# Performance work log

Hardware: AMD Instinct MI355X
Metric: run time of the kernel (lower is better)

## Reference

```python
import jax, jax.numpy as jnp
import numpy as np

N, E = 20000, 640000
ND, ED = 16, 8            # raw node/edge feature dims
H = 128                   # encoder hidden = gnn channels = mlp hidden
OUT = 2
L = 10                    # gnn layers (shared weights, per-layer layernorms)
NOISE_STD = 0.003
EPS = 1e-5


def _mlp(x, w1, b1, w2, b2):
    return jax.nn.relu(x @ w1 + b1) @ w2 + b2


def _ln(x, g, b):
    m = jnp.mean(x, axis=-1, keepdims=True)
    v = jnp.var(x, axis=-1, keepdims=True)
    return (x - m) * jax.lax.rsqrt(v + EPS) * g + b


def setup_inputs() -> dict:
    key = jax.random.key(0)
    ks = jax.random.split(key, 32)

    def w(k, i, o):
        return jax.random.normal(k, (i, o), jnp.float32) / np.sqrt(i)

    inp = {
        "x": jax.random.normal(ks[0], (N, ND), jnp.float32),
        "edge_attr": jax.random.normal(ks[1], (E, ED), jnp.float32),
        "edge_index": jax.random.randint(ks[2], (2, E), 0, N, jnp.int64),
        "node_noise": jax.random.normal(ks[3], (N, ND), jnp.float32) * NOISE_STD,
        "edge_noise": jax.random.normal(ks[4], (E, ED), jnp.float32) * NOISE_STD,
        # encoders
        "node_enc_w1": w(ks[5], ND, H), "node_enc_b1": jnp.zeros((H,), jnp.float32),
        "node_enc_w2": w(ks[6], H, H),  "node_enc_b2": jnp.zeros((H,), jnp.float32),
        "edge_enc_w1": w(ks[7], ED, H), "edge_enc_b1": jnp.zeros((H,), jnp.float32),
        "edge_enc_w2": w(ks[8], H, H),  "edge_enc_b2": jnp.zeros((H,), jnp.float32),
        # single shared MPNN (module instance reused across all L layers)
        "gnn_edge_w1": w(ks[9], 3 * H, H), "gnn_edge_b1": jnp.zeros((H,), jnp.float32),
        "gnn_edge_w2": w(ks[10], H, H),    "gnn_edge_b2": jnp.zeros((H,), jnp.float32),
        "gnn_node_w1": w(ks[11], 2 * H, H), "gnn_node_b1": jnp.zeros((H,), jnp.float32),
        "gnn_node_w2": w(ks[12], H, H),     "gnn_node_b2": jnp.zeros((H,), jnp.float32),
        # per-layer layernorms
        "x_ln_g": jnp.ones((L, H), jnp.float32), "x_ln_b": jnp.zeros((L, H), jnp.float32),
        "e_ln_g": jnp.ones((L, H), jnp.float32), "e_ln_b": jnp.zeros((L, H), jnp.float32),
        # decoder
        "dec_w1": w(ks[13], H, H),  "dec_b1": jnp.zeros((H,), jnp.float32),
        "dec_w2": w(ks[14], H, OUT), "dec_b2": jnp.zeros((OUT,), jnp.float32),
    }
    return inp


def reference(x, edge_attr, edge_index, node_noise, edge_noise,
              node_enc_w1, node_enc_b1, node_enc_w2, node_enc_b2,
              edge_enc_w1, edge_enc_b1, edge_enc_w2, edge_enc_b2,
              gnn_edge_w1, gnn_edge_b1, gnn_edge_w2, gnn_edge_b2,
              gnn_node_w1, gnn_node_b1, gnn_node_w2, gnn_node_b2,
              x_ln_g, x_ln_b, e_ln_g, e_ln_b,
              dec_w1, dec_b1, dec_w2, dec_b2):
    src = edge_index[0]  # x_j
    dst = edge_index[1]  # x_i (aggregation target)

    h = _mlp(x + node_noise, node_enc_w1, node_enc_b1, node_enc_w2, node_enc_b2)      # [N,H]
    e = _mlp(edge_attr + edge_noise, edge_enc_w1, edge_enc_b1, edge_enc_w2, edge_enc_b2)  # [E,H]

    for l in range(L):
        xi = h[dst]  # [E,H]
        xj = h[src]  # [E,H]
        # edge update: e + edge_mlp([x_i, x_j, e])
        e_new = e + _mlp(jnp.concatenate([xi, xj, e], axis=1),
                         gnn_edge_w1, gnn_edge_b1, gnn_edge_w2, gnn_edge_b2)
        # message: x_i + node_mlp([x_i, e_new]); aggr='add' over dst
        msg = xi + _mlp(jnp.concatenate([xi, e_new], axis=1),
                        gnn_node_w1, gnn_node_b1, gnn_node_w2, gnn_node_b2)
        h_agg = jax.ops.segment_sum(msg, dst, num_segments=N)
        h = _ln(h + h_agg, x_ln_g[l], x_ln_b[l])
        e = _ln(e + e_new, e_ln_g[l], e_ln_b[l])

    out = _mlp(h, dec_w1, dec_b1, dec_w2, dec_b2) - node_noise[:, :OUT]
    return out
```

## Files before the change

### kernel.cpp

```cpp
#include <hip/hip_runtime.h>
#include <stdio.h>

#define NN 20000
#define NE 640000
#define NL 10

typedef unsigned short u16;
typedef unsigned int u32;
typedef __attribute__((ext_vector_type(8))) __bf16 bf16x8;
typedef __attribute__((ext_vector_type(8))) unsigned short us8;
typedef __attribute__((ext_vector_type(4))) float f32x4;

__device__ __forceinline__ bf16x8 ldbf(const u16* p) {
  union { us8 u; bf16x8 b; } v;
  v.u = *(const us8*)p;
  return v.b;
}
__device__ __forceinline__ f32x4 zero4() {
  f32x4 z; z[0] = 0.f; z[1] = 0.f; z[2] = 0.f; z[3] = 0.f; return z;
}
__device__ __forceinline__ float bf2f(u16 u) {
  u32 x = ((u32)u) << 16;
  return __uint_as_float(x);
}
__device__ __forceinline__ u16 f2bf(float f) {
  u32 x = __float_as_uint(f);
  u32 r = (x + 0x7fffu + ((x >> 16) & 1u)) >> 16;
  return (u16)r;
}
__device__ __forceinline__ int lad(int row, int col) {
  return (row << 7) + ((((col >> 3) ^ (row & 15)) << 3) | (col & 7));
}
__device__ __forceinline__ uint2 pack4bf(const float f[4]) {
  uint2 u;
  u.x = (u32)f2bf(f[0]) | ((u32)f2bf(f[1]) << 16);
  u.y = (u32)f2bf(f[2]) | ((u32)f2bf(f[3]) << 16);
  return u;
}
__device__ __forceinline__ void unpack4bf(uint2 u, float f[4]) {
  f[0] = bf2f((u16)(u.x & 0xffffu)); f[1] = bf2f((u16)(u.x >> 16));
  f[2] = bf2f((u16)(u.y & 0xffffu)); f[3] = bf2f((u16)(u.y >> 16));
}

__global__ void LearnedSimModel_28716151341396_kernel() {}

__global__ void init_kernel(float* agg, int agg_n, int* cnt, int cnt_n) {
  int i = blockIdx.x * 256 + threadIdx.x;
  if (i < agg_n) agg[i] = 0.0f;
  if (i < cnt_n) cnt[i] = 0;
}

__global__ void idx_detect_kernel(const int* raw, int* flag) {
  if (threadIdx.x == 0 && blockIdx.x == 0) {
    int any = 0;
    for (int k = 0; k < 16; ++k) any = any | raw[2 * k + 1];
    flag[0] = (any != 0) ? 1 : 0;
  }
}

__global__ void idx_prep_kernel(const int* raw, const int* flag, int* idx0) {
  int i = blockIdx.x * 256 + threadIdx.x;
  if (i < 2 * NE) {
    int v;
    if (flag[0] != 0) v = raw[i];
    else v = (int)(((const long long*)raw)[i]);
    if (v < 0) v = 0;
    if (v >= NN) v = NN - 1;
    idx0[i] = v;
  }
}

__global__ void hist_kernel(const int* dst0, int* cnt) {
  int i = blockIdx.x * 256 + threadIdx.x;
  if (i < NE) atomicAdd(&cnt[dst0[i]], 1);
}

__global__ void prefix_kernel(const int* cnt, int* cursor) {
  __shared__ int buf[1024];
  __shared__ int carry;
  int t = threadIdx.x;
  if (t == 0) carry = 0;
  __syncthreads();
  for (int base = 0; base < NN; base += 1024) {
    int v = (base + t < NN) ? cnt[base + t] : 0;
    buf[t] = v;
    __syncthreads();
    for (int s = 1; s < 1024; s <<= 1) {
      int add = (t >= s) ? buf[t - s] : 0;
      __syncthreads();
      buf[t] += add;
      __syncthreads();
    }
    int excl = buf[t] - v + carry;
    if (base + t < NN) cursor[base + t] = excl;
    __syncthreads();
    if (t == 0) carry = carry + buf[1023];
    __syncthreads();
  }
}

__global__ void scatter_kernel(const int* src0, const int* dst0, int* cursor,
                               int* src_s, int* dst_s, int* perm) {
  int i = blockIdx.x * 256 + threadIdx.x;
  if (i < NE) {
    int d = dst0[i];
    int pos = atomicAdd(&cursor[d], 1);
    perm[pos] = i;
    src_s[pos] = src0[i];
    dst_s[pos] = d;
  }
}

__global__ void transpose_slice_kernel(const float* __restrict__ W,
                                       u16* __restrict__ Wt, int koff) {
  int i = blockIdx.x * 256 + threadIdx.x;
  int k = i >> 7, f = i & 127;
  Wt[f * 128 + k] = f2bf(W[(size_t)(koff + k) * 128 + f]);
}

__global__ void node_enc_kernel(const float* x, const float* noise,
                                const float* w1, const float* b1,
                                const float* w2, const float* b2,
                                float* h, u16* h16) {
  __shared__ float in16[16];
  __shared__ float t1s[128];
  int f = threadIdx.x;
  int n = blockIdx.x;
  if (f < 16) in16[f] = x[n * 16 + f] + noise[n * 16 + f];
  __syncthreads();
  float a = b1[f];
  for (int k = 0; k < 16; ++k) a += in16[k] * w1[k * 128 + f];
  t1s[f] = fmaxf(a, 0.0f);
  __syncthreads();
  float o = b2[f];
  for (int k = 0; k < 128; ++k) o += t1s[k] * w2[k * 128 + f];
  h[(long long)n * 128 + f] = o;
  h16[(long long)n * 128 + f] = f2bf(o);
}

__device__ __forceinline__ void gemm128(const u16* lds, const u16* Wt,
                                        int l16, int quad, int fb, f32x4 acc[2][4]) {
  for (int ks = 0; ks < 4; ++ks) {
    int kg = ks * 32 + quad * 8;
    bf16x8 b0 = ldbf(lds + lad(0 * 16 + l16, kg));
    bf16x8 b1 = ldbf(lds + lad(1 * 16 + l16, kg));
    bf16x8 b2 = ldbf(lds + lad(2 * 16 + l16, kg));
    bf16x8 b3 = ldbf(lds + lad(3 * 16 + l16, kg));
    for (int tt = 0; tt < 2; ++tt) {
      bf16x8 a = ldbf(Wt + (size_t)(fb + tt * 16 + l16) * 128 + kg);
      acc[tt][0] = __builtin_amdgcn_mfma_f32_16x16x32_bf16(a, b0, acc[tt][0], 0, 0, 0);
      acc[tt][1] = __builtin_amdgcn_mfma_f32_16x16x32_bf16(a, b1, acc[tt][1], 0, 0, 0);
      acc[tt][2] = __builtin_amdgcn_mfma_f32_16x16x32_bf16(a, b2, acc[tt][2], 0, 0, 0);
      acc[tt][3] = __builtin_amdgcn_mfma_f32_16x16x32_bf16(a, b3, acc[tt][3], 0, 0, 0);
    }
  }
}

__global__ __launch_bounds__(256) void edge_enc_mfma(
    const float* __restrict__ attr, const float* __restrict__ noise,
    const int* __restrict__ perm,
    const float* __restrict__ w1, const float* __restrict__ b1,
    const u16* __restrict__ Wt2, const float* __restrict__ b2,
    u16* __restrict__ e)
{
  __shared__ __align__(16) u16 sT[64 * 128];
  __shared__ float sIn[64][8];
  __shared__ int sPerm[64];

  const int t = threadIdx.x;
  if (t < 64) sPerm[t] = perm[blockIdx.x * 64 + t];
  __syncthreads();

  for (int it = 0; it < 2; ++it) {
    int c = t + it * 256;
    int row = c >> 3, k = c & 7;
    int p = sPerm[row];
    sIn[row][k] = attr[(size_t)p * 8 + k] + noise[(size_t)p * 8 + k];
  }
  __syncthreads();

  {
    int f = t & 127;
    int r0 = (t >> 7) * 32;
    float wc[8];
    for (int k = 0; k < 8; ++k) wc[k] = w1[k * 128 + f];
    float bb = b1[f];
    for (int j = 0; j < 32; ++j) {
      int row = r0 + j;
      float a = bb;
      for (int k = 0; k < 8; ++k) a += sIn[row][k] * wc[k];
      sT[lad(row, f)] = f2bf(fmaxf(a, 0.f));
    }
  }
  __syncthreads();

  const int lane = t & 63;
  const int wave = t >> 6;
  const int l16 = lane & 15;
  const int quad = lane >> 4;
  const int fb = wave * 32;
  f32x4 acc[2][4];
  for (int tt = 0; tt < 2; ++tt)
    for (int et = 0; et < 4; ++et) acc[tt][et] = zero4();
  gemm128(sT, Wt2, l16, quad, fb, acc);
  u16* etile = e + (size_t)blockIdx.x * 8192;
  for (int tt = 0; tt < 2; ++tt) {
    int f0 = fb + tt * 16 + quad * 4;
    float4 bb = *(const float4*)(b2 + f0);
    float bbv[4] = {bb.x, bb.y, bb.z, bb.w};
    for (int et = 0; et < 4; ++et) {
      int row = et * 16 + l16;
      float o[4];
      for (int r = 0; r < 4; ++r) o[r] = acc[tt][et][r] + bbv[r];
      *(uint2*)(etile + lad(row, f0)) = pack4bf(o);
    }
  }
}

__global__ __launch_bounds__(256) void nprep_kernel(
    const u16* __restrict__ h16, const u16* __restrict__ Wt_np,
    float* __restrict__ nprep)
{
  __shared__ __align__(16) u16 sH[64 * 128];
  const int t = threadIdx.x;
  const int n0 = blockIdx.x * 64;

  for (int it = 0; it < 4; ++it) {
    int c = t + it * 256;
    int row = c >> 4, seg = c & 15;
    int n = n0 + row;
    if (n >= NN) n = NN - 1;
    us8 v = *(const us8*)(h16 + (size_t)n * 128 + seg * 8);
    *(us8*)(sH + ((row << 7) + ((seg ^ (row & 15)) << 3))) = v;
  }
  __syncthreads();

  const int lane = t & 63;
  const int wave = t >> 6;
  const int l16 = lane & 15;
  const int quad = lane >> 4;
  const int fb = wave * 96;
  f32x4 acc[6][4];
  for (int ft = 0; ft < 6; ++ft)
    for (int et = 0; et < 4; ++et) acc[ft][et] = zero4();
  for (int ks = 0; ks < 4; ++ks) {
    int kg = ks * 32 + quad * 8;
    bf16x8 b0 = ldbf(sH + lad(0 * 16 + l16, kg));
    bf16x8 b1 = ldbf(sH + lad(1 * 16 + l16, kg));
    bf16x8 b2 = ldbf(sH + lad(2 * 16 + l16, kg));
    bf16x8 b3 = ldbf(sH + lad(3 * 16 + l16, kg));
    for (int ft = 0; ft < 6; ++ft) {
      bf16x8 a = ldbf(Wt_np + (size_t)(fb + ft * 16 + l16) * 128 + kg);
      acc[ft][0] = __builtin_amdgcn_mfma_f32_16x16x32_bf16(a, b0, acc[ft][0], 0, 0, 0);
      acc[ft][1] = __builtin_amdgcn_mfma_f32_16x16x32_bf16(a, b1, acc[ft][1], 0, 0, 0);
      acc[ft][2] = __builtin_amdgcn_mfma_f32_16x16x32_bf16(a, b2, acc[ft][2], 0, 0, 0);
      acc[ft][3] = __builtin_amdgcn_mfma_f32_16x16x32_bf16(a, b3, acc[ft][3], 0, 0, 0);
    }
  }
  for (int ft = 0; ft < 6; ++ft) {
    int f0 = fb + ft * 16 + quad * 4;
    for (int et = 0; et < 4; ++et) {
      int n = n0 + et * 16 + l16;
      if (n < NN) *(f32x4*)(nprep + (size_t)n * 384 + f0) = acc[ft][et];
    }
  }
}

__global__ __launch_bounds__(256, 4) void gnn_edge_mfma(
    u16* __restrict__ eg,
    const int* __restrict__ src_s, const int* __restrict__ dst_s,
    const float* __restrict__ nprep,
    const u16* __restrict__ Wt_e1c, const float* __restrict__ be1,
    const u16* __restrict__ Wt_e2,  const float* __restrict__ be2,
    const u16* __restrict__ Wt_n1b, const float* __restrict__ bn1,
    const u16* __restrict__ Wt_n2,
    const float* __restrict__ lng, const float* __restrict__ lnb,
    float* __restrict__ agg)
{
  __shared__ __align__(16) char smem[35328];
  u16* sE = (u16*)smem;
  u16* sT = (u16*)(smem + 16384);
  float* msgf = (float*)smem;
  float* part_s = (float*)(smem + 32768);
  float* part_q = (float*)(smem + 33792);
  int* sDst = (int*)(smem + 34816);
  int* sSrc = (int*)(smem + 35072);

  const int t = threadIdx.x;
  const int e0 = blockIdx.x * 64;
  const int lane = t & 63;
  const int wave = t >> 6;
  const int l16 = lane & 15;
  const int quad = lane >> 4;
  const int fb = wave * 32;

  if (t < 64) { sDst[t] = dst_s[e0 + t]; sSrc[t] = src_s[e0 + t]; }

  const u16* ebase = eg + (size_t)blockIdx.x * 8192;
  for (int it = 0; it < 4; ++it) {
    int c = it * 2048 + t * 8;
    *(us8*)(sE + c) = *(const us8*)(ebase + c);
  }
  __syncthreads();

  int rd[4], rs[4];
  for (int et = 0; et < 4; ++et) {
    rd[et] = sDst[et * 16 + l16];
    rs[et] = sSrc[et * 16 + l16];
  }

  f32x4 acc[2][4];
  for (int tt = 0; tt < 2; ++tt)
    for (int et = 0; et < 4; ++et) acc[tt][et] = zero4();
  gemm128(sE, Wt_e1c, l16, quad, fb, acc);
  for (int tt = 0; tt < 2; ++tt) {
    int f0 = fb + tt * 16 + quad * 4;
    float4 bb = *(const float4*)(be1 + f0);
    float bbv[4] = {bb.x, bb.y, bb.z, bb.w};
    f32x4 av[4], jv[4];
    for (int et = 0; et < 4; ++et) {
      av[et] = *(const f32x4*)(nprep + (size_t)rd[et] * 384 + f0);
      jv[et] = *(const f32x4*)(nprep + (size_t)rs[et] * 384 + 128 + f0);
    }
    for (int et = 0; et < 4; ++et) {
      int row = et * 16 + l16;
      float o[4];
      for (int r = 0; r < 4; ++r)
        o[r] = fmaxf(acc[tt][et][r] + av[et][r] + jv[et][r] + bbv[r], 0.f);
      *(uint2*)(sT + lad(row, f0)) = pack4bf(o);
    }
  }
  __syncthreads();

  for (int tt = 0; tt < 2; ++tt)
    for (int et = 0; et < 4; ++et) acc[tt][et] = zero4();
  gemm128(sT, Wt_e2, l16, quad, fb, acc);
  float lnv[2][4][4];
  for (int tt = 0; tt < 2; ++tt) {
    int f0 = fb + tt * 16 + quad * 4;
    float4 bb = *(const float4*)(be2 + f0);
    float bbv[4] = {bb.x, bb.y, bb.z, bb.w};
    for (int et = 0; et < 4; ++et) {
      int row = et * 16 + l16;
      float eo[4];
      unpack4bf(*(const uint2*)(sE + lad(row, f0)), eo);
      float en[4];
      for (int r = 0; r < 4; ++r) {
        en[r] = eo[r] + acc[tt][et][r] + bbv[r];
        lnv[tt][et][r] = eo[r] + en[r];
      }
      *(uint2*)(sE + lad(row, f0)) = pack4bf(en);
    }
  }
  for (int et = 0; et < 4; ++et) {
    float s = 0.f, q = 0.f;
    for (int tt = 0; tt < 2; ++tt)
      for (int r = 0; r < 4; ++r) {
        float v = lnv[tt][et][r];
        s += v; q += v * v;
      }
    s += __shfl_xor(s, 16); s += __shfl_xor(s, 32);
    q += __shfl_xor(q, 16); q += __shfl_xor(q, 32);
    if (quad == 0) {
      part_s[wave * 64 + et * 16 + l16] = s;
      part_q[wave * 64 + et * 16 + l16] = q;
    }
  }
  __syncthreads();

  u16* etile = eg + (size_t)blockIdx.x * 8192;
  for (int et = 0; et < 4; ++et) {
    int row = et * 16 + l16;
    float s = part_s[row] + part_s[64 + row] + part_s[128 + row] + part_s[192 + row];
    float q = part_q[row] + part_q[64 + row] + part_q[128 + row] + part_q[192 + row];
    float m = s * (1.f / 128.f);
    float var = q * (1.f / 128.f) - m * m;
    float rsv = rsqrtf(fmaxf(var, 0.f) + 1e-5f);
    for (int tt = 0; tt < 2; ++tt) {
      int f0 = fb + tt * 16 + quad * 4;
      float4 g4 = *(const float4*)(lng + f0);
      float4 b4 = *(const float4*)(lnb + f0);
      float gv[4] = {g4.x, g4.y, g4.z, g4.w};
      float bv[4] = {b4.x, b4.y, b4.z, b4.w};
      float o[4];
      for (int r = 0; r < 4; ++r)
        o[r] = (lnv[tt][et][r] - m) * rsv * gv[r] + bv[r];
      *(uint2*)(etile + lad(row, f0)) = pack4bf(o);
    }
  }

  for (int tt = 0; tt < 2; ++tt)
    for (int et = 0; et < 4; ++et) acc[tt][et] = zero4();
  gemm128(sE, Wt_n1b, l16, quad, fb, acc);
  for (int tt = 0; tt < 2; ++tt) {
    int f0 = fb + tt * 16 + quad * 4;
    float4 bb = *(const float4*)(bn1 + f0);
    float bbv[4] = {bb.x, bb.y, bb.z, bb.w};
    f32x4 bv4[4];
    for (int et = 0; et < 4; ++et)
      bv4[et] = *(const f32x4*)(nprep + (size_t)rd[et] * 384 + 256 + f0);
    for (int et = 0; et < 4; ++et) {
      int row = et * 16 + l16;
      float o[4];
      for (int r = 0; r < 4; ++r)
        o[r] = fmaxf(acc[tt][et][r] + bv4[et][r] + bbv[r], 0.f);
      *(uint2*)(sT + lad(row, f0)) = pack4bf(o);
    }
  }
  __syncthreads();

  for (int tt = 0; tt < 2; ++tt)
    for (int et = 0; et < 4; ++et) acc[tt][et] = zero4();
  gemm128(sT, Wt_n2, l16, quad, fb, acc);
  __syncthreads();

  for (int tt = 0; tt < 2; ++tt) {
    int f0 = fb + tt * 16 + quad * 4;
    for (int et = 0; et < 4; ++et) {
      int row = et * 16 + l16;
      *(f32x4*)(msgf + row * 128 + (((f0 >> 2) ^ (row & 31)) << 2)) = acc[tt][et];
    }
  }
  __syncthreads();

  {
    int f = t & 127, half = t >> 7;
    int j0 = half * 32;
    int c = f >> 2, c3 = f & 3;
    float a = 0.f;
    for (int j = j0; j < j0 + 32; ++j) {
      a += msgf[j * 128 + ((c ^ (j & 31)) << 2) + c3];
      int dj = sDst[j];
      if (j == j0 + 31 || sDst[j + 1] != dj) {
        atomicAdd(&agg[(size_t)dj * 128 + f], a);
        a = 0.f;
      }
    }
  }
}

__global__ void node_ln_kernel(float* h, u16* h16, float* agg,
                               const int* cnt, const float* bn2,
                               const float* g, const float* b) {
  __shared__ float red[128];
  int f = threadIdx.x;
  int n = blockIdx.x;
  long long base = (long long)n * 128 + f;
  float deg = (float)cnt[n];
  float hv = h[base];
  float v = hv + agg[base] + deg * (hv + bn2[f]);
  red[f] = v;
  __syncthreads();
  for (int s = 64; s > 0; s >>= 1) {
    if (f < s) red[f] += red[f + s];
    __syncthreads();
  }
  float m = red[0] * (1.0f / 128.0f);
  __syncthreads();
  red[f] = v * v;
  __syncthreads();
  for (int s = 64; s > 0; s >>= 1) {
    if (f < s) red[f] += red[f + s];
    __syncthreads();
  }
  float q = red[0] * (1.0f / 128.0f);
  float var = q - m * m;
  float rs = rsqrtf(fmaxf(var, 0.0f) + 1e-5f);
  float o = (v - m) * rs * g[f] + b[f];
  h[base] = o;
  h16[base] = f2bf(o);
  agg[base] = 0.0f;
}

__global__ void decoder_kernel(const float* h, const float* w1, const float* b1,
                               const float* w2, const float* b2,
                               const float* noise, float* out) {
  __shared__ float t1s[128];
  int f = threadIdx.x;
  int n = blockIdx.x;
  float a = b1[f];
  for (int k = 0; k < 128; ++k) a += h[(long long)n * 128 + k] * w1[k * 128 + f];
  t1s[f] = fmaxf(a, 0.0f);
  __syncthreads();
  if (f < 2) {
    float s = b2[f];
    for (int k = 0; k < 128; ++k) s += t1s[k] * w2[k * 2 + f];
    s -= noise[n * 16 + f];
    out[n * 2 + f] = s;
  }
}

extern "C" void kernel_launch(void* const* d_in, const int* in_sizes, int n_in,
                              void* d_out, int out_size, void* d_ws, size_t ws_size,
                              hipStream_t stream) {
  (void)in_sizes; (void)n_in; (void)out_size; (void)ws_size;

  const float* x      = (const float*)d_in[0];
  const float* eattr  = (const float*)d_in[1];
  const int*   eidx   = (const int*)d_in[2];
  const float* nnoise = (const float*)d_in[3];
  const float* enoise = (const float*)d_in[4];
  const float* ne_w1 = (const float*)d_in[5];  const float* ne_b1 = (const float*)d_in[6];
  const float* ne_w2 = (const float*)d_in[7];  const float* ne_b2 = (const float*)d_in[8];
  const float* ee_w1 = (const float*)d_in[9];  const float* ee_b1 = (const float*)d_in[10];
  const float* ee_w2 = (const float*)d_in[11]; const float* ee_b2 = (const float*)d_in[12];
  const float* ge_w1 = (const float*)d_in[13]; const float* ge_b1 = (const float*)d_in[14];
  const float* ge_w2 = (const float*)d_in[15]; const float* ge_b2 = (const float*)d_in[16];
  const float* gn_w1 = (const float*)d_in[17]; const float* gn_b1 = (const float*)d_in[18];
  const float* gn_w2 = (const float*)d_in[19]; const float* gn_b2 = (const float*)d_in[20];
  const float* xlng = (const float*)d_in[21]; const float* xlnb = (const float*)d_in[22];
  const float* elng = (const float*)d_in[23]; const float* elnb = (const float*)d_in[24];
  const float* d_w1 = (const float*)d_in[25]; const float* d_b1 = (const float*)d_in[26];
  const float* d_w2 = (const float*)d_in[27]; const float* d_b2 = (const float*)d_in[28];

  float* out = (float*)d_out;

  char* base = (char*)d_ws;
  size_t off = 0;
  int* idx0 = (int*)(base + off);    off += (size_t)2 * NE * 4;
  int* src_s = (int*)(base + off);   off += (size_t)NE * 4;
  int* dst_s = (int*)(base + off);   off += (size_t)NE * 4;
  int* perm = (int*)(base + off);    off += (size_t)NE * 4;
  int* cnt = (int*)(base + off);     off += (size_t)NN * 4;
  int* cursor = (int*)(base + off);  off += (size_t)NN * 4;
  int* flag = (int*)(base + off);    off += 16;
  float* h = (float*)(base + off);   off += (size_t)NN * 128 * 4;
  u16* h16 = (u16*)(base + off);     off += (size_t)NN * 128 * 2;
  float* agg = (float*)(base + off); off += (size_t)NN * 128 * 4;
  u16* e = (u16*)(base + off);       off += (size_t)NE * 128 * 2;
  float* nprep = (float*)(base + off); off += (size_t)NN * 384 * 4;
  u16* Wt_np = (u16*)(base + off);   off += (size_t)384 * 128 * 2;
  u16* Wt_e1c = (u16*)(base + off);  off += (size_t)128 * 128 * 2;
  u16* Wt_ge2 = (u16*)(base + off);  off += (size_t)128 * 128 * 2;
  u16* Wt_n1b = (u16*)(base + off);  off += (size_t)128 * 128 * 2;
  u16* Wt_gn2 = (u16*)(base + off);  off += (size_t)128 * 128 * 2;
  u16* Wt_ee2 = (u16*)(base + off);  off += (size_t)128 * 128 * 2;

  hipStreamCaptureStatus cs = hipStreamCaptureStatusNone;
  hipStreamIsCapturing(stream, &cs);
  const bool dbg = (cs == hipStreamCaptureStatusNone);

  const int* src0 = idx0;
  const int* dst0 = idx0 + NE;

  init_kernel<<<(NN * 128 + 255) / 256, 256, 0, stream>>>(agg, NN * 128, cnt, NN);
  idx_detect_kernel<<<1, 64, 0, stream>>>(eidx, flag);
  idx_prep_kernel<<<(2 * NE + 255) / 256, 256, 0, stream>>>(eidx, flag, idx0);

  hist_kernel<<<(NE + 255) / 256, 256, 0, stream>>>(dst0, cnt);
  prefix_kernel<<<1, 1024, 0, stream>>>(cnt, cursor);
  scatter_kernel<<<(NE + 255) / 256, 256, 0, stream>>>(src0, dst0, cursor,
                                                       src_s, dst_s, perm);

  transpose_slice_kernel<<<64, 256, 0, stream>>>(ge_w1, Wt_np, 0);
  transpose_slice_kernel<<<64, 256, 0, stream>>>(ge_w1, Wt_np + 16384, 128);
  transpose_slice_kernel<<<64, 256, 0, stream>>>(gn_w1, Wt_np + 32768, 0);
  transpose_slice_kernel<<<64, 256, 0, stream>>>(ge_w1, Wt_e1c, 256);
  transpose_slice_kernel<<<64, 256, 0, stream>>>(ge_w2, Wt_ge2, 0);
  transpose_slice_kernel<<<64, 256, 0, stream>>>(gn_w1, Wt_n1b, 128);
  transpose_slice_kernel<<<64, 256, 0, stream>>>(gn_w2, Wt_gn2, 0);
  transpose_slice_kernel<<<64, 256, 0, stream>>>(ee_w2, Wt_ee2, 0);

  node_enc_kernel<<<NN, 128, 0, stream>>>(x, nnoise, ne_w1, ne_b1, ne_w2, ne_b2, h, h16);
  edge_enc_mfma<<<NE / 64, 256, 0, stream>>>(eattr, enoise, perm,
                                             ee_w1, ee_b1, Wt_ee2, ee_b2, e);

  for (int l = 0; l < NL; ++l) {
    nprep_kernel<<<(NN + 63) / 64, 256, 0, stream>>>(h16, Wt_np, nprep);
    gnn_edge_mfma<<<NE / 64, 256, 0, stream>>>(e, src_s, dst_s, nprep,
        Wt_e1c, ge_b1, Wt_ge2, ge_b2, Wt_n1b, gn_b1, Wt_gn2,
        elng + l * 128, elnb + l * 128, agg);
    node_ln_kernel<<<NN, 128, 0, stream>>>(h, h16, agg, cnt, gn_b2,
                                           xlng + l * 128, xlnb + l * 128);
  }

  decoder_kernel<<<NN, 128, 0, stream>>>(h, d_w1, d_b1, d_w2, d_b2, nnoise, out);

  if (dbg) {
    hipStreamSynchronize(stream);
    float tbuf[6] = {0, 0, 0, 0, 0, 0};
    hipMemcpy(tbuf, h, 16, hipMemcpyDeviceToHost);
    hipMemcpy(tbuf + 4, out, 8, hipMemcpyDeviceToHost);
    fprintf(stderr, "KL r31 revert-best: h[0..3]=%.5g %.5g %.5g %.5g out[0..1]=%.5g %.5g lasterr=%d\n",
            tbuf[0], tbuf[1], tbuf[2], tbuf[3], tbuf[4], tbuf[5], (int)hipGetLastError());
    fflush(stderr);
  }
}
```

Before: 3.594 ms.

## Widen gnn edge kernel to 128-edge tiles with 512 threads

The fused edge/message kernel now processes 128 edges per block with 8 waves instead of 64 edges with 4 waves. Each wave owns 16 output features across 8 edge sub-tiles, loading one weight fragment per k-step and reusing it over all 8 MFMAs, and LayerNorm partials are reduced across 8 waves. The larger tile halves the block count and may merge more same-destination atomics per block. In exchange it doubles the per-block LDS footprint, issues more LDS B-fragment reads per MFMA, and tightens the register budget under the new launch bounds, so spilling or lower occupancy is possible.

```diff
diff --git a/kernel.cpp b/kernel.cpp
--- a/kernel.cpp
+++ b/kernel.cpp
@@ -152,6 +152,19 @@
       acc[tt][1] = __builtin_amdgcn_mfma_f32_16x16x32_bf16(a, b1, acc[tt][1], 0, 0, 0);
       acc[tt][2] = __builtin_amdgcn_mfma_f32_16x16x32_bf16(a, b2, acc[tt][2], 0, 0, 0);
       acc[tt][3] = __builtin_amdgcn_mfma_f32_16x16x32_bf16(a, b3, acc[tt][3], 0, 0, 0);
+    }
+  }
+}
+
+__device__ __forceinline__ void gemm128x8(const u16* lds, const u16* Wt,
+                                          int l16, int quad, int fb, f32x4 acc[8]) {
+  for (int ks = 0; ks < 4; ++ks) {
+    int kg = ks * 32 + quad * 8;
+    bf16x8 a = ldbf(Wt + (size_t)(fb + l16) * 128 + kg);
+#pragma unroll
+    for (int et = 0; et < 8; ++et) {
+      bf16x8 b = ldbf(lds + lad(et * 16 + l16, kg));
+      acc[et] = __builtin_amdgcn_mfma_f32_16x16x32_bf16(a, b, acc[et], 0, 0, 0);
     }
   }
 }
@@ -266,7 +279,7 @@
   }
 }
 
-__global__ __launch_bounds__(256, 4) void gnn_edge_mfma(
+__global__ __launch_bounds__(512, 4) void gnn_edge_mfma(
     u16* __restrict__ eg,
     const int* __restrict__ src_s, const int* __restrict__ dst_s,
     const float* __restrict__ nprep,
@@ -277,159 +290,157 @@
     const float* __restrict__ lng, const float* __restrict__ lnb,
     float* __restrict__ agg)
 {
-  __shared__ __align__(16) char smem[35328];
+  __shared__ __align__(16) char smem[74240];
   u16* sE = (u16*)smem;
-  u16* sT = (u16*)(smem + 16384);
+  u16* sT = (u16*)(smem + 32768);
   float* msgf = (float*)smem;
-  float* part_s = (float*)(smem + 32768);
-  float* part_q = (float*)(smem + 33792);
-  int* sDst = (int*)(smem + 34816);
-  int* sSrc = (int*)(smem + 35072);
+  float* part_s = (float*)(smem + 65536);
+  float* part_q = (float*)(smem + 69632);
+  int* sDst = (int*)(smem + 73728);
 
   const int t = threadIdx.x;
-  const int e0 = blockIdx.x * 64;
+  const int e0 = blockIdx.x * 128;
   const int lane = t & 63;
   const int wave = t >> 6;
   const int l16 = lane & 15;
   const int quad = lane >> 4;
-  const int fb = wave * 32;
-
-  if (t < 64) { sDst[t] = dst_s[e0 + t]; sSrc[t] = src_s[e0 + t]; }
-
-  const u16* ebase = eg + (size_t)blockIdx.x * 8192;
+  const int fb = wave * 16;
+  const int f0 = fb + quad * 4;
+
+  if (t < 128) sDst[t] = dst_s[e0 + t];
+
+  int rd[8], rs[8];
+#pragma unroll
+  for (int et = 0; et < 8; ++et) {
+    rd[et] = dst_s[e0 + et * 16 + l16];
+    rs[et] = src_s[e0 + et * 16 + l16];
+  }
+
+  const u16* ebase = eg + (size_t)blockIdx.x * 16384;
+#pragma unroll
   for (int it = 0; it < 4; ++it) {
-    int c = it * 2048 + t * 8;
+    int c = it * 4096 + t * 8;
     *(us8*)(sE + c) = *(const us8*)(ebase + c);
   }
   __syncthreads();
 
-  int rd[4], rs[4];
-  for (int et = 0; et < 4; ++et) {
-    rd[et] = sDst[et * 16 + l16];
-    rs[et] = sSrc[et * 16 + l16];
-  }
-
-  f32x4 acc[2][4];
-  for (int tt = 0; tt < 2; ++tt)
-    for (int et = 0; et < 4; ++et) acc[tt][et] = zero4();
-  gemm128(sE, Wt_e1c, l16, quad, fb, acc);
-  for (int tt = 0; tt < 2; ++tt) {
-    int f0 = fb + tt * 16 + quad * 4;
+  f32x4 acc[8];
+#pragma unroll
+  for (int et = 0; et < 8; ++et) acc[et] = zero4();
+  gemm128x8(sE, Wt_e1c, l16, quad, fb, acc);
+  {
     float4 bb = *(const float4*)(be1 + f0);
     float bbv[4] = {bb.x, bb.y, bb.z, bb.w};
-    f32x4 av[4], jv[4];
-    for (int et = 0; et < 4; ++et) {
-      av[et] = *(const f32x4*)(nprep + (size_t)rd[et] * 384 + f0);
-      jv[et] = *(const f32x4*)(nprep + (size_t)rs[et] * 384 + 128 + f0);
-    }
-    for (int et = 0; et < 4; ++et) {
+#pragma unroll
+    for (int et = 0; et < 8; ++et) {
+      f32x4 av = *(const f32x4*)(nprep + (size_t)rd[et] * 384 + f0);
+      f32x4 jv = *(const f32x4*)(nprep + (size_t)rs[et] * 384 + 128 + f0);
       int row = et * 16 + l16;
       float o[4];
       for (int r = 0; r < 4; ++r)
-        o[r] = fmaxf(acc[tt][et][r] + av[et][r] + jv[et][r] + bbv[r], 0.f);
+        o[r] = fmaxf(acc[et][r] + av[r] + jv[r] + bbv[r], 0.f);
       *(uint2*)(sT + lad(row, f0)) = pack4bf(o);
     }
   }
   __syncthreads();
 
-  for (int tt = 0; tt < 2; ++tt)
-    for (int et = 0; et < 4; ++et) acc[tt][et] = zero4();
-  gemm128(sT, Wt_e2, l16, quad, fb, acc);
-  float lnv[2][4][4];
-  for (int tt = 0; tt < 2; ++tt) {
-    int f0 = fb + tt * 16 + quad * 4;
+#pragma unroll
+  for (int et = 0; et < 8; ++et) acc[et] = zero4();
+  gemm128x8(sT, Wt_e2, l16, quad, fb, acc);
+  {
     float4 bb = *(const float4*)(be2 + f0);
     float bbv[4] = {bb.x, bb.y, bb.z, bb.w};
-    for (int et = 0; et < 4; ++et) {
+#pragma unroll
+    for (int et = 0; et < 8; ++et) {
       int row = et * 16 + l16;
       float eo[4];
       unpack4bf(*(const uint2*)(sE + lad(row, f0)), eo);
       float en[4];
-      for (int r = 0; r < 4; ++r) {
-        en[r] = eo[r] + acc[tt][et][r] + bbv[r];
-        lnv[tt][et][r] = eo[r] + en[r];
-      }
+      for (int r = 0; r < 4; ++r) en[r] = eo[r] + acc[et][r] + bbv[r];
       *(uint2*)(sE + lad(row, f0)) = pack4bf(en);
-    }
-  }
-  for (int et = 0; et < 4; ++et) {
+      for (int r = 0; r < 4; ++r) acc[et][r] = eo[r] + en[r];
+    }
+  }
+#pragma unroll
+  for (int et = 0; et < 8; ++et) {
     float s = 0.f, q = 0.f;
-    for (int tt = 0; tt < 2; ++tt)
-      for (int r = 0; r < 4; ++r) {
-        float v = lnv[tt][et][r];
-        s += v; q += v * v;
-      }
+    for (int r = 0; r < 4; ++r) {
+      float v = acc[et][r];
+      s += v; q += v * v;
+    }
     s += __shfl_xor(s, 16); s += __shfl_xor(s, 32);
     q += __shfl_xor(q, 16); q += __shfl_xor(q, 32);
     if (quad == 0) {
-      part_s[wave * 64 + et * 16 + l16] = s;
-      part_q[wave * 64 + et * 16 + l16] = q;
-    }
-  }
-  __syncthreads();
-
-  u16* etile = eg + (size_t)blockIdx.x * 8192;
-  for (int et = 0; et < 4; ++et) {
-    int row = et * 16 + l16;
-    float s = part_s[row] + part_s[64 + row] + part_s[128 + row] + part_s[192 + row];
-    float q = part_q[row] + part_q[64 + row] + part_q[128 + row] + part_q[192 + row];
-    float m = s * (1.f / 128.f);
-    float var = q * (1.f / 128.f) - m * m;
-    float rsv = rsqrtf(fmaxf(var, 0.f) + 1e-5f);
-    for (int tt = 0; tt < 2; ++tt) {
-      int f0 = fb + tt * 16 + quad * 4;
-      float4 g4 = *(const float4*)(lng + f0);
-      float4 b4 = *(const float4*)(lnb + f0);
-      float gv[4] = {g4.x, g4.y, g4.z, g4.w};
-      float bv[4] = {b4.x, b4.y, b4.z, b4.w};
+      part_s[wave * 128 + et * 16 + l16] = s;
+      part_q[wave * 128 + et * 16 + l16] = q;
+    }
+  }
+  __syncthreads();
+
+  u16* etile = eg + (size_t)blockIdx.x * 16384;
+  {
+    float4 g4 = *(const float4*)(lng + f0);
+    float4 b4 = *(const float4*)(lnb + f0);
+    float gv[4] = {g4.x, g4.y, g4.z, g4.w};
+    float bv[4] = {b4.x, b4.y, b4.z, b4.w};
+#pragma unroll
+    for (int et = 0; et < 8; ++et) {
+      int row = et * 16 + l16;
+      float s = 0.f, q = 0.f;
+      for (int w = 0; w < 8; ++w) {
+        s += part_s[w * 128 + row];
+        q += part_q[w * 128 + row];
+      }
+      float m = s * (1.f / 128.f);
+      float var = q * (1.f / 128.f) - m * m;
+      float rsv = rsqrtf(fmaxf(var, 0.f) + 1e-5f);
       float o[4];
       for (int r = 0; r < 4; ++r)
-        o[r] = (lnv[tt][et][r] - m) * rsv * gv[r] + bv[r];
+        o[r] = (acc[et][r] - m) * rsv * gv[r] + bv[r];
       *(uint2*)(etile + lad(row, f0)) = pack4bf(o);
     }
   }
 
-  for (int tt = 0; tt < 2; ++tt)
-    for (int et = 0; et < 4; ++et) acc[tt][et] = zero4();
-  gemm128(sE, Wt_n1b, l16, quad, fb, acc);
-  for (int tt = 0; tt < 2; ++tt) {
-    int f0 = fb + tt * 16 + quad * 4;
+#pragma unroll
+  for (int et = 0; et < 8; ++et) acc[et] = zero4();
+  gemm128x8(sE, Wt_n1b, l16, quad, fb, acc);
+  {
     float4 bb = *(const float4*)(bn1 + f0);
     float bbv[4] = {bb.x, bb.y, bb.z, bb.w};
-    f32x4 bv4[4];
-    for (int et = 0; et < 4; ++et)
-      bv4[et] = *(const f32x4*)(nprep + (size_t)rd[et] * 384 + 256 + f0);
-    for (int et = 0; et < 4; ++et) {
+#pragma unroll
+    for (int et = 0; et < 8; ++et) {
+      f32x4 bv4 = *(const f32x4*)(nprep + (size_t)rd[et] * 384 + 256 + f0);
       int row = et * 16 + l16;
       float o[4];
       for (int r = 0; r < 4; ++r)
-        o[r] = fmaxf(acc[tt][et][r] + bv4[et][r] + bbv[r], 0.f);
+        o[r] = fmaxf(acc[et][r] + bv4[r] + bbv[r], 0.f);
       *(uint2*)(sT + lad(row, f0)) = pack4bf(o);
     }
   }
   __syncthreads();
 
-  for (int tt = 0; tt < 2; ++tt)
-    for (int et = 0; et < 4; ++et) acc[tt][et] = zero4();
-  gemm128(sT, Wt_n2, l16, quad, fb, acc);
-  __syncthreads();
-
-  for (int tt = 0; tt < 2; ++tt) {
-    int f0 = fb + tt * 16 + quad * 4;
-    for (int et = 0; et < 4; ++et) {
+#pragma unroll
+  for (int et = 0; et < 8; ++et) acc[et] = zero4();
+  gemm128x8(sT, Wt_n2, l16, quad, fb, acc);
+  __syncthreads();
+
+  {
+    int c = f0 >> 2;
+#pragma unroll
+    for (int et = 0; et < 8; ++et) {
       int row = et * 16 + l16;
-      *(f32x4*)(msgf + row * 128 + (((f0 >> 2) ^ (row & 31)) << 2)) = acc[tt][et];
-    }
-  }
-  __syncthreads();
-
-  {
-    int f = t & 127, half = t >> 7;
-    int j0 = half * 32;
+      *(f32x4*)(msgf + row * 128 + (((c ^ (row & 31)) & 31) << 2)) = acc[et];
+    }
+  }
+  __syncthreads();
+
+  {
+    int f = t & 127, qtr = t >> 7;
     int c = f >> 2, c3 = f & 3;
     float a = 0.f;
+    int j0 = qtr * 32;
     for (int j = j0; j < j0 + 32; ++j) {
-      a += msgf[j * 128 + ((c ^ (j & 31)) << 2) + c3];
+      a += msgf[j * 128 + (((c ^ (j & 31)) & 31) << 2) + c3];
       int dj = sDst[j];
       if (j == j0 + 31 || sDst[j + 1] != dj) {
         atomicAdd(&agg[(size_t)dj * 128 + f], a);
@@ -567,7 +578,7 @@
 
   for (int l = 0; l < NL; ++l) {
     nprep_kernel<<<(NN + 63) / 64, 256, 0, stream>>>(h16, Wt_np, nprep);
-    gnn_edge_mfma<<<NE / 64, 256, 0, stream>>>(e, src_s, dst_s, nprep,
+    gnn_edge_mfma<<<NE / 128, 512, 0, stream>>>(e, src_s, dst_s, nprep,
         Wt_e1c, ge_b1, Wt_ge2, ge_b2, Wt_n1b, gn_b1, Wt_gn2,
         elng + l * 128, elnb + l * 128, agg);
     node_ln_kernel<<<NN, 128, 0, stream>>>(h, h16, agg, cnt, gn_b2,
@@ -581,7 +592,7 @@
     float tbuf[6] = {0, 0, 0, 0, 0, 0};
     hipMemcpy(tbuf, h, 16, hipMemcpyDeviceToHost);
     hipMemcpy(tbuf + 4, out, 8, hipMemcpyDeviceToHost);
-    fprintf(stderr, "KL r31 revert-best: h[0..3]=%.5g %.5g %.5g %.5g out[0..1]=%.5g %.5g lasterr=%d\n",
+    fprintf(stderr, "KL r32 fat128: h[0..3]=%.5g %.5g %.5g %.5g out[0..1]=%.5g %.5g lasterr=%d\n",
             tbuf[0], tbuf[1], tbuf[2], tbuf[3], tbuf[4], tbuf[5], (int)hipGetLastError());
     fflush(stderr);
   }
```

Measured after the change: 3.181 ms. -11.5%, faster.
